# Performance work log

Measured on AMD Instinct MI355X. Metric: run time of the kernel, lower is better.

The kernel has to match this reference:

```python
import jax, jax.numpy as jnp
import numpy as np

B, N, E = 64, 256, 2048          # graphs per batch, nodes per subgraph, edges per subgraph
V, D, H = 50000, 128, 4          # vocab_size, hidden_dim, heads
NEG_SLOPE = 0.2                  # PyG GATConv default LeakyReLU slope


def setup_inputs() -> dict:
    key = jax.random.key(0)
    ks = jax.random.split(key, 16)
    s = 0.05
    return {
        "neighbors_node1": jax.random.randint(ks[0], (B, N), 0, V),
        "neighbors_node2": jax.random.randint(ks[1], (B, N), 0, V),
        "adj1": jax.random.randint(ks[2], (B, 2, E), 0, N),
        "adj2": jax.random.randint(ks[3], (B, 2, E), 0, N),
        "emb": jax.random.normal(ks[4], (V + 1, D), jnp.float32) * 0.02,
        # GATConv 1: lin weight [H*D, D], att_src/att_dst [H, D], bias [D] (concat=False)
        "W1": jax.random.normal(ks[5], (H * D, D), jnp.float32) * s,
        "att_src1": jax.random.normal(ks[6], (H, D), jnp.float32) * s,
        "att_dst1": jax.random.normal(ks[7], (H, D), jnp.float32) * s,
        "b1": jnp.zeros((D,), jnp.float32),
        # GATConv 2
        "W2": jax.random.normal(ks[8], (H * D, D), jnp.float32) * s,
        "att_src2": jax.random.normal(ks[9], (H, D), jnp.float32) * s,
        "att_dst2": jax.random.normal(ks[10], (H, D), jnp.float32) * s,
        "b2": jnp.zeros((D,), jnp.float32),
        # final MLP: Linear(2D -> 1)
        "mlp_w": jax.random.normal(ks[11], (1, 2 * D), jnp.float32) * s,
        "mlp_b": jnp.zeros((1,), jnp.float32),
    }


def _gat_conv(x, edge_index, W, a_src, a_dst, bias):
    """PyG GATConv, concat=False (mean over heads), with self-loops.
    x: [N, D] node features; edge_index: [2, E] (row=src j, col=dst i)."""
    xh = (x @ W.T).reshape(N, H, D)                      # [N, H, D]
    loop = jnp.arange(N)
    src = jnp.concatenate([edge_index[0], loop])          # [E+N]
    dst = jnp.concatenate([edge_index[1], loop])
    asrc = jnp.einsum('nhd,hd->nh', xh, a_src)            # [N, H]
    adst = jnp.einsum('nhd,hd->nh', xh, a_dst)
    e = jax.nn.leaky_relu(asrc[src] + adst[dst], NEG_SLOPE)   # [E+N, H]
    # softmax over incoming edges of each dst node
    m = jax.ops.segment_max(e, dst, num_segments=N)
    ex = jnp.exp(e - m[dst])
    denom = jax.ops.segment_sum(ex, dst, num_segments=N)
    alpha = ex / denom[dst]                               # [E+N, H]
    out = jax.ops.segment_sum(xh[src] * alpha[:, :, None], dst, num_segments=N)  # [N, H, D]
    return out.mean(axis=1) + bias                        # [N, D]


def reference(neighbors_node1, neighbors_node2, adj1, adj2, emb,
              W1, att_src1, att_dst1, b1,
              W2, att_src2, att_dst2, b2,
              mlp_w, mlp_b):
    f1 = jax.vmap(lambda n, ei: _gat_conv(emb[n], ei, W1, att_src1, att_dst1, b1))(
        neighbors_node1, adj1)                            # [B, N, D]
    f2 = jax.vmap(lambda n, ei: _gat_conv(emb[n], ei, W2, att_src2, att_dst2, b2))(
        neighbors_node2, adj2)
    feats = jnp.concatenate([f1[:, 0], f2[:, 0]], axis=-1)  # center node of each subgraph -> [B, 2D]
    return (feats @ mlp_w.T + mlp_b)[:, 0]                # [B]
```

## Files before the change

### kernel.cpp

```cpp
#include <hip/hip_runtime.h>
#include <hip/hip_bf16.h>

#define Bg 64
#define Nn 256
#define Ee 2048
#define Dd 128
#define Hh 4
#define MAXJ 40
#define RS 132

__device__ __forceinline__ float bf2f(unsigned short u) {
    return __uint_as_float(((unsigned)u) << 16);
}

__global__ __launch_bounds__(1024) void gat_fused_kernel(
    const int* nn1, const int* nn2, const int* adj1, const int* adj2,
    const void* emb,
    const void* W1, const void* as1, const void* ad1, const void* b1,
    const void* W2, const void* as2, const void* ad2, const void* b2,
    const void* mlpw, const void* mlpb, void* out)
{
    __shared__ float s_wv[24 * RS];
    __shared__ float s_rows[2 * MAXJ * RS];
    __shared__ float s_red4[4];
    __shared__ int   s_srcj[2][MAXJ];
    __shared__ int   s_gid[2 * MAXJ];
    __shared__ int   s_cnt[2];
    __shared__ int   s_f32;
    __shared__ float s_ps[2 * MAXJ * Hh], s_pm[2 * MAXJ * Hh];
    __shared__ float s_pd[2 * Hh], s_hval[2 * Hh], s_bdot[2];

    const int tid = threadIdx.x;
    const int b = blockIdx.x;

    if (tid == 0) { s_f32 = 0; s_cnt[0] = 0; s_cnt[1] = 0; }
    __syncthreads();

    if (tid < 128) {
        float v = bf2f(((const unsigned short*)W1)[tid]);
        bool bad = !(v > -64.f && v < 64.f);
        if (__any(bad) && (tid & 63) == 0) atomicOr(&s_f32, 1);
    }
    __syncthreads();
    const int f32 = s_f32;

    {
        const int l = tid >> 9, i = tid & 511;
        const int* adjp = (l ? adj2 : adj1) + (long)b * 2 * Ee;
        int4 d4 = ((const int4*)(adjp + Ee))[i];
        int base = i * 4;
        if (d4.x == 0) { int p = atomicAdd(&s_cnt[l], 1); if (p < MAXJ - 1) s_srcj[l][p] = adjp[base + 0]; }
        if (d4.y == 0) { int p = atomicAdd(&s_cnt[l], 1); if (p < MAXJ - 1) s_srcj[l][p] = adjp[base + 1]; }
        if (d4.z == 0) { int p = atomicAdd(&s_cnt[l], 1); if (p < MAXJ - 1) s_srcj[l][p] = adjp[base + 2]; }
        if (d4.w == 0) { int p = atomicAdd(&s_cnt[l], 1); if (p < MAXJ - 1) s_srcj[l][p] = adjp[base + 3]; }
    }

    {
        const int s = tid >> 7;
        const int k = tid & 127;
        const int l = s >> 2;
        const int h = s & 3;
        const void* Wp  = l ? W2 : W1;
        const void* asp = l ? as2 : as1;
        const void* adp = l ? ad2 : ad1;
        float a0 = 0.f, a1 = 0.f, a2 = 0.f;
        if (f32) {
            const float* Wf = (const float*)Wp + (long)h * Dd * Dd + k;
            const float* pa = (const float*)asp + h * Dd;
            const float* pb = (const float*)adp + h * Dd;
            const float* pm = (const float*)mlpw + l * Dd;
            #pragma unroll 8
            for (int d = 0; d < Dd; ++d) {
                float w = Wf[(long)d * Dd];
                a0 += pa[d] * w; a1 += pb[d] * w; a2 += pm[d] * w;
            }
        } else {
            const unsigned short* Wb = (const unsigned short*)Wp + (long)h * Dd * Dd + k;
            const unsigned short* pa = (const unsigned short*)asp + h * Dd;
            const unsigned short* pb = (const unsigned short*)adp + h * Dd;
            const unsigned short* pm = (const unsigned short*)mlpw + l * Dd;
            #pragma unroll 8
            for (int d = 0; d < Dd; ++d) {
                float w = bf2f(Wb[(long)d * Dd]);
                a0 += bf2f(pa[d]) * w; a1 += bf2f(pb[d]) * w; a2 += bf2f(pm[d]) * w;
            }
        }
        s_wv[((l * 3 + 0) * 4 + h) * RS + k] = a0;
        s_wv[((l * 3 + 1) * 4 + h) * RS + k] = a1;
        s_wv[((l * 3 + 2) * 4 + h) * RS + k] = a2;
    }

    if (tid < 256) {
        const int l = tid >> 7, d = tid & 127;
        const void* bias = l ? b2 : b1;
        float bv, mv;
        if (f32) {
            bv = ((const float*)bias)[d];
            mv = ((const float*)mlpw)[l * Dd + d];
        } else {
            bv = bf2f(((const unsigned short*)bias)[d]);
            mv = bf2f(((const unsigned short*)mlpw)[l * Dd + d]);
        }
        float p = bv * mv;
        #pragma unroll
        for (int off = 32; off > 0; off >>= 1) p += __shfl_down(p, off);
        if ((tid & 63) == 0) s_red4[tid >> 6] = p;
    }
    __syncthreads();

    if (tid < 2) {
        float a = s_red4[2 * tid] + s_red4[2 * tid + 1];
        if (tid == 0)
            a += f32 ? ((const float*)mlpb)[0]
                     : bf2f(((const unsigned short*)mlpb)[0]);
        s_bdot[tid] = a;
        int c = s_cnt[tid];
        if (c > MAXJ - 1) c = MAXJ - 1;
        s_srcj[tid][c] = 0;
        s_cnt[tid] = c + 1;
    }
    __syncthreads();
    const int cnt0 = s_cnt[0], cnt1 = s_cnt[1];
    const int tot = cnt0 + cnt1;

    if (tid < 2 * MAXJ) {
        int l = tid / MAXJ, j = tid % MAXJ;
        int cl = l ? cnt1 : cnt0;
        if (j < cl) {
            const int* nodes = l ? nn2 : nn1;
            s_gid[l ? (cnt0 + j) : j] = nodes[b * Nn + s_srcj[l][j]];
        }
    }
    __syncthreads();

    for (int idx = tid; idx < tot * 32; idx += 1024) {
        int j = idx >> 5, k4 = (idx & 31) * 4;
        long gid = s_gid[j];
        float4 f;
        if (f32) {
            f = ((const float4*)emb)[gid * 32 + (k4 >> 2)];
        } else {
            ushort4 u = *(const ushort4*)((const unsigned short*)emb + gid * Dd + k4);
            f.x = bf2f(u.x); f.y = bf2f(u.y); f.z = bf2f(u.z); f.w = bf2f(u.w);
        }
        *(float4*)&s_rows[j * RS + k4] = f;
    }
    __syncthreads();

    const int ntask = tot * 8 + 8;
    for (int task = tid; task < ntask; task += 1024) {
        int j, h, t, l;
        if (task < tot * 8) {
            j = task >> 3; h = (task >> 1) & 3; t = (task & 1) ? 2 : 0;
            l = (j < cnt0) ? 0 : 1;
        } else {
            int z = task - tot * 8;
            l = z >> 2; h = z & 3; t = 1;
            j = l ? (tot - 1) : (cnt0 - 1);
        }
        const float* wrow = s_wv + ((l * 3 + t) * 4 + h) * RS;
        const float* row  = s_rows + j * RS;
        float acc = 0.f;
        #pragma unroll 8
        for (int k = 0; k < Dd; ++k) acc += row[k] * wrow[k];
        if (task < tot * 8) {
            if (task & 1) s_pm[j * Hh + h] = acc;
            else          s_ps[j * Hh + h] = acc;
        } else {
            s_pd[(l << 2) | h] = acc;
        }
    }
    __syncthreads();

    if (tid < 8) {
        int l = tid >> 2, h = tid & 3;
        int j0 = l ? cnt0 : 0;
        int j1 = l ? tot : cnt0;
        float pd = s_pd[tid], m = -1e30f;
        for (int j = j0; j < j1; ++j) {
            float e = s_ps[j * Hh + h] + pd;
            e = (e >= 0.f) ? e : 0.2f * e;
            s_ps[j * Hh + h] = e;
            if (e > m) m = e;
        }
        float den = 0.f, num = 0.f;
        for (int j = j0; j < j1; ++j) {
            float ex = expf(s_ps[j * Hh + h] - m);
            den += ex;
            num += ex * s_pm[j * Hh + h];
        }
        s_hval[tid] = num / den;
    }
    __syncthreads();
    if (tid == 0) {
        float r = 0.25f * (s_hval[0] + s_hval[1] + s_hval[2] + s_hval[3]) + s_bdot[0]
                + 0.25f * (s_hval[4] + s_hval[5] + s_hval[6] + s_hval[7]) + s_bdot[1];
        if (f32) ((float*)out)[b] = r;
        else     ((__hip_bfloat16*)out)[b] = __float2bfloat16(r);
    }
}

extern "C" void kernel_launch(void* const* d_in, const int* in_sizes, int n_in,
                              void* d_out, int out_size, void* d_ws, size_t ws_size,
                              hipStream_t stream) {
    const int* nn1  = (const int*)d_in[0];
    const int* nn2  = (const int*)d_in[1];
    const int* adj1 = (const int*)d_in[2];
    const int* adj2 = (const int*)d_in[3];

    gat_fused_kernel<<<Bg, 1024, 0, stream>>>(
        nn1, nn2, adj1, adj2,
        d_in[4],
        d_in[5],   d_in[6],   d_in[7],
        d_in[8],
        d_in[9],   d_in[10],  d_in[11],
        d_in[12],
        d_in[13],  d_in[14],
        d_out);
}
```

Before: 117.7 us.

## Split weight-vector projections into a precompute kernel shared by all graph blocks

Moves the W·(att_src, att_dst, mlp_w) projections and the bias dot products out of the per-graph kernel into a separate 8-block kernel that writes them to workspace. The main kernel then loads the small result instead of each of the 64 blocks re-reading both 128x128x4 weight matrices. It also stages the node index arrays in shared memory, widens bf16 embedding loads to 16 bytes, and halves the block size to 512. This adds a second launch and a global round-trip for the precomputed vectors.

```diff
diff --git a/kernel.cpp b/kernel.cpp
--- a/kernel.cpp
+++ b/kernel.cpp
@@ -13,16 +13,118 @@
     return __uint_as_float(((unsigned)u) << 16);
 }
 
-__global__ __launch_bounds__(1024) void gat_fused_kernel(
-    const int* nn1, const int* nn2, const int* adj1, const int* adj2,
-    const void* emb,
+__global__ __launch_bounds__(256) void precompute_kernel(
     const void* W1, const void* as1, const void* ad1, const void* b1,
     const void* W2, const void* as2, const void* ad2, const void* b2,
-    const void* mlpw, const void* mlpb, void* out)
+    const void* mlpw, const void* mlpb, float* wv)
+{
+    __shared__ float s_av[3 * Dd];
+    __shared__ float s_part[8 * 3 * Dd];
+    __shared__ float s_red[2];
+    __shared__ int   s_f32;
+
+    const int tid = threadIdx.x;
+    const int x = blockIdx.x;
+    const int l = x >> 2, h = x & 3;
+
+    if (tid < 64) {
+        float v = bf2f(((const unsigned short*)W1)[tid]);
+        bool bad = !(v > -64.f && v < 64.f);
+        unsigned long long m = __ballot(bad);
+        if (tid == 0) s_f32 = (m != 0ull) ? 1 : 0;
+    }
+    __syncthreads();
+    const int f32 = s_f32;
+
+    for (int i = tid; i < 3 * Dd; i += 256) {
+        int t = i >> 7, d = i & 127;
+        const void* p; long off;
+        if (t == 0)      { p = l ? as2 : as1; off = (long)h * Dd + d; }
+        else if (t == 1) { p = l ? ad2 : ad1; off = (long)h * Dd + d; }
+        else             { p = mlpw;          off = (long)l * Dd + d; }
+        s_av[i] = f32 ? ((const float*)p)[off]
+                      : bf2f(((const unsigned short*)p)[off]);
+    }
+    __syncthreads();
+
+    {
+        const int kc = (tid & 31) * 4;
+        const int d0 = (tid >> 5) * 16;
+        float acc[3][4] = {};
+        if (f32) {
+            const float* Wf = (const float*)(l ? W2 : W1) + (long)h * Dd * Dd;
+            #pragma unroll
+            for (int dd = 0; dd < 16; ++dd) {
+                int d = d0 + dd;
+                float4 w = *(const float4*)(Wf + (long)d * Dd + kc);
+                #pragma unroll
+                for (int t = 0; t < 3; ++t) {
+                    float a = s_av[t * Dd + d];
+                    acc[t][0] += a * w.x; acc[t][1] += a * w.y;
+                    acc[t][2] += a * w.z; acc[t][3] += a * w.w;
+                }
+            }
+        } else {
+            const unsigned short* Wb =
+                (const unsigned short*)(l ? W2 : W1) + (long)h * Dd * Dd;
+            #pragma unroll
+            for (int dd = 0; dd < 16; ++dd) {
+                int d = d0 + dd;
+                ushort4 u = *(const ushort4*)(Wb + (long)d * Dd + kc);
+                float wx = bf2f(u.x), wy = bf2f(u.y);
+                float wz = bf2f(u.z), ww = bf2f(u.w);
+                #pragma unroll
+                for (int t = 0; t < 3; ++t) {
+                    float a = s_av[t * Dd + d];
+                    acc[t][0] += a * wx; acc[t][1] += a * wy;
+                    acc[t][2] += a * wz; acc[t][3] += a * ww;
+                }
+            }
+        }
+        const int dg = tid >> 5;
+        #pragma unroll
+        for (int t = 0; t < 3; ++t)
+            *(float4*)&s_part[(dg * 3 + t) * Dd + kc] =
+                make_float4(acc[t][0], acc[t][1], acc[t][2], acc[t][3]);
+    }
+    __syncthreads();
+
+    for (int i = tid; i < 3 * Dd; i += 256) {
+        int t = i >> 7, k = i & 127;
+        float s = 0.f;
+        #pragma unroll
+        for (int g = 0; g < 8; ++g) s += s_part[(g * 3 + t) * Dd + k];
+        wv[((l * 3 + t) * 4 + h) * Dd + k] = s;
+    }
+
+    if (h == 0) {
+        float p = 0.f;
+        if (tid < 128) {
+            const void* bias = l ? b2 : b1;
+            float bv = f32 ? ((const float*)bias)[tid]
+                           : bf2f(((const unsigned short*)bias)[tid]);
+            p = bv * s_av[2 * Dd + tid];
+        }
+        #pragma unroll
+        for (int off = 32; off > 0; off >>= 1) p += __shfl_down(p, off);
+        if (tid == 0 || tid == 64) s_red[tid >> 6] = p;
+        __syncthreads();
+        if (tid == 0) {
+            float a = s_red[0] + s_red[1];
+            if (l == 0) a += f32 ? ((const float*)mlpb)[0]
+                                 : bf2f(((const unsigned short*)mlpb)[0]);
+            wv[3072 + l] = a;
+        }
+    }
+}
+
+__global__ __launch_bounds__(512) void gat_main_kernel(
+    const int* nn1, const int* nn2, const int* adj1, const int* adj2,
+    const void* emb, const void* W1, const float* wv, void* out)
 {
     __shared__ float s_wv[24 * RS];
     __shared__ float s_rows[2 * MAXJ * RS];
-    __shared__ float s_red4[4];
+    __shared__ int   s_nodes[2][Nn];
     __shared__ int   s_srcj[2][MAXJ];
     __shared__ int   s_gid[2 * MAXJ];
     __shared__ int   s_cnt[2];
@@ -33,19 +135,18 @@
     const int tid = threadIdx.x;
     const int b = blockIdx.x;
 
-    if (tid == 0) { s_f32 = 0; s_cnt[0] = 0; s_cnt[1] = 0; }
-    __syncthreads();
-
-    if (tid < 128) {
+    if (tid == 0) { s_cnt[0] = 0; s_cnt[1] = 0; }
+    if (tid < 64) {
         float v = bf2f(((const unsigned short*)W1)[tid]);
         bool bad = !(v > -64.f && v < 64.f);
-        if (__any(bad) && (tid & 63) == 0) atomicOr(&s_f32, 1);
+        unsigned long long m = __ballot(bad);
+        if (tid == 0) s_f32 = (m != 0ull) ? 1 : 0;
     }
     __syncthreads();
     const int f32 = s_f32;
 
-    {
-        const int l = tid >> 9, i = tid & 511;
+    for (int v = tid; v < 2 * (Ee / 4); v += 512) {
+        int l = v >> 9, i = v & 511;
         const int* adjp = (l ? adj2 : adj1) + (long)b * 2 * Ee;
         int4 d4 = ((const int4*)(adjp + Ee))[i];
         int base = i * 4;
@@ -54,66 +155,19 @@
         if (d4.z == 0) { int p = atomicAdd(&s_cnt[l], 1); if (p < MAXJ - 1) s_srcj[l][p] = adjp[base + 2]; }
         if (d4.w == 0) { int p = atomicAdd(&s_cnt[l], 1); if (p < MAXJ - 1) s_srcj[l][p] = adjp[base + 3]; }
     }
-
     {
-        const int s = tid >> 7;
-        const int k = tid & 127;
-        const int l = s >> 2;
-        const int h = s & 3;
-        const void* Wp  = l ? W2 : W1;
-        const void* asp = l ? as2 : as1;
-        const void* adp = l ? ad2 : ad1;
-        float a0 = 0.f, a1 = 0.f, a2 = 0.f;
-        if (f32) {
-            const float* Wf = (const float*)Wp + (long)h * Dd * Dd + k;
-            const float* pa = (const float*)asp + h * Dd;
-            const float* pb = (const float*)adp + h * Dd;
-            const float* pm = (const float*)mlpw + l * Dd;
-            #pragma unroll 8
-            for (int d = 0; d < Dd; ++d) {
-                float w = Wf[(long)d * Dd];
-                a0 += pa[d] * w; a1 += pb[d] * w; a2 += pm[d] * w;
-            }
-        } else {
-            const unsigned short* Wb = (const unsigned short*)Wp + (long)h * Dd * Dd + k;
-            const unsigned short* pa = (const unsigned short*)asp + h * Dd;
-            const unsigned short* pb = (const unsigned short*)adp + h * Dd;
-            const unsigned short* pm = (const unsigned short*)mlpw + l * Dd;
-            #pragma unroll 8
-            for (int d = 0; d < Dd; ++d) {
-                float w = bf2f(Wb[(long)d * Dd]);
-                a0 += bf2f(pa[d]) * w; a1 += bf2f(pb[d]) * w; a2 += bf2f(pm[d]) * w;
-            }
-        }
-        s_wv[((l * 3 + 0) * 4 + h) * RS + k] = a0;
-        s_wv[((l * 3 + 1) * 4 + h) * RS + k] = a1;
-        s_wv[((l * 3 + 2) * 4 + h) * RS + k] = a2;
-    }
-
-    if (tid < 256) {
-        const int l = tid >> 7, d = tid & 127;
-        const void* bias = l ? b2 : b1;
-        float bv, mv;
-        if (f32) {
-            bv = ((const float*)bias)[d];
-            mv = ((const float*)mlpw)[l * Dd + d];
-        } else {
-            bv = bf2f(((const unsigned short*)bias)[d]);
-            mv = bf2f(((const unsigned short*)mlpw)[l * Dd + d]);
-        }
-        float p = bv * mv;
-        #pragma unroll
-        for (int off = 32; off > 0; off >>= 1) p += __shfl_down(p, off);
-        if ((tid & 63) == 0) s_red4[tid >> 6] = p;
-    }
+        int l = tid >> 8, n = tid & 255;
+        s_nodes[l][n] = (l ? nn2 : nn1)[b * Nn + n];
+    }
+    for (int i = tid; i < 768; i += 512) {
+        float4 f = ((const float4*)wv)[i];
+        int el = i * 4, row = el >> 7, k = el & 127;
+        *(float4*)&s_wv[row * RS + k] = f;
+    }
+    if (tid < 2) s_bdot[tid] = wv[3072 + tid];
     __syncthreads();
 
     if (tid < 2) {
-        float a = s_red4[2 * tid] + s_red4[2 * tid + 1];
-        if (tid == 0)
-            a += f32 ? ((const float*)mlpb)[0]
-                     : bf2f(((const unsigned short*)mlpb)[0]);
-        s_bdot[tid] = a;
         int c = s_cnt[tid];
         if (c > MAXJ - 1) c = MAXJ - 1;
         s_srcj[tid][c] = 0;
@@ -126,29 +180,34 @@
     if (tid < 2 * MAXJ) {
         int l = tid / MAXJ, j = tid % MAXJ;
         int cl = l ? cnt1 : cnt0;
-        if (j < cl) {
-            const int* nodes = l ? nn2 : nn1;
-            s_gid[l ? (cnt0 + j) : j] = nodes[b * Nn + s_srcj[l][j]];
-        }
-    }
-    __syncthreads();
-
-    for (int idx = tid; idx < tot * 32; idx += 1024) {
-        int j = idx >> 5, k4 = (idx & 31) * 4;
-        long gid = s_gid[j];
-        float4 f;
-        if (f32) {
-            f = ((const float4*)emb)[gid * 32 + (k4 >> 2)];
-        } else {
-            ushort4 u = *(const ushort4*)((const unsigned short*)emb + gid * Dd + k4);
-            f.x = bf2f(u.x); f.y = bf2f(u.y); f.z = bf2f(u.z); f.w = bf2f(u.w);
-        }
-        *(float4*)&s_rows[j * RS + k4] = f;
+        if (j < cl) s_gid[l ? (cnt0 + j) : j] = s_nodes[l][s_srcj[l][j]];
+    }
+    __syncthreads();
+
+    if (f32) {
+        for (int idx = tid; idx < tot * 32; idx += 512) {
+            int j = idx >> 5, k4 = (idx & 31) << 2;
+            long gid = s_gid[j];
+            float4 f = ((const float4*)emb)[gid * 32 + (k4 >> 2)];
+            *(float4*)&s_rows[j * RS + k4] = f;
+        }
+    } else {
+        for (int idx = tid; idx < tot * 16; idx += 512) {
+            int j = idx >> 4, k8 = (idx & 15) << 3;
+            long gid = s_gid[j];
+            uint4 u = *(const uint4*)((const unsigned short*)emb + gid * Dd + k8);
+            float4 f0 = make_float4(bf2f(u.x & 0xffff), bf2f(u.x >> 16),
+                                    bf2f(u.y & 0xffff), bf2f(u.y >> 16));
+            float4 f1 = make_float4(bf2f(u.z & 0xffff), bf2f(u.z >> 16),
+                                    bf2f(u.w & 0xffff), bf2f(u.w >> 16));
+            *(float4*)&s_rows[j * RS + k8] = f0;
+            *(float4*)&s_rows[j * RS + k8 + 4] = f1;
+        }
     }
     __syncthreads();
 
     const int ntask = tot * 8 + 8;
-    for (int task = tid; task < ntask; task += 1024) {
+    for (int task = tid; task < ntask; task += 512) {
         int j, h, t, l;
         if (task < tot * 8) {
             j = task >> 3; h = (task >> 1) & 3; t = (task & 1) ? 2 : 0;
@@ -207,14 +266,15 @@
     const int* nn2  = (const int*)d_in[1];
     const int* adj1 = (const int*)d_in[2];
     const int* adj2 = (const int*)d_in[3];
-
-    gat_fused_kernel<<<Bg, 1024, 0, stream>>>(
-        nn1, nn2, adj1, adj2,
-        d_in[4],
+    float* wv = (float*)d_ws;
+
+    precompute_kernel<<<8, 256, 0, stream>>>(
         d_in[5],   d_in[6],   d_in[7],
         d_in[8],
         d_in[9],   d_in[10],  d_in[11],
         d_in[12],
-        d_in[13],  d_in[14],
-        d_out);
-}
+        d_in[13],  d_in[14],  wv);
+
+    gat_main_kernel<<<Bg, 512, 0, stream>>>(
+        nn1, nn2, adj1, adj2, d_in[4] , d_in[5] , wv, d_out);
+}
```

After: 104.3 us (median of 2 runs). 1.13x faster.
